# Kernel tuning notes

Hardware: AMD Instinct MI355X
Metric: run time of the kernel (lower is better)

The kernel has to match this reference:

```python
import jax, jax.numpy as jnp
import numpy as np


def hard_sig(x):
    # Keras hard_sigmoid: relu6(x + 3) / 6
    return jnp.clip(x / 6.0 + 0.5, 0.0, 1.0)


def conv2d(x, k):
    # x: (B,H,W,Cin), k: (kh,kw,Cin,Cout), SAME padding, stride 1
    return jax.lax.conv_general_dilated(x, k, (1, 1), 'SAME',
                                        dimension_numbers=('NHWC', 'HWIO', 'NHWC'))


def convlstm_layer(xs, Wk, Uk, b):
    # xs: (B,T,H,W,Cin); Wk: (kh,kw,Cin,4F); Uk: (kh,kw,F,4F); b: (4F,)
    B, T, H, W, _ = xs.shape
    F = b.shape[0] // 4
    h0 = jnp.zeros((B, H, W, F), xs.dtype)
    c0 = jnp.zeros((B, H, W, F), xs.dtype)
    xs_t = jnp.moveaxis(xs, 1, 0)  # (T,B,H,W,Cin)

    def step(carry, xt):
        h, c = carry
        z = conv2d(xt, Wk) + conv2d(h, Uk) + b
        zi, zf, zg, zo = jnp.split(z, 4, axis=-1)  # Keras gate order i,f,c,o
        i = hard_sig(zi)
        f = hard_sig(zf)
        o = hard_sig(zo)
        c_new = f * c + i * jax.nn.relu(zg)      # activation='relu'
        h_new = o * jax.nn.relu(c_new)
        return (h_new, c_new), h_new

    _, hs = jax.lax.scan(step, (h0, c0), xs_t)
    return jnp.moveaxis(hs, 0, 1)  # (B,T,H,W,F)


def batchnorm(x, gamma, beta, mean, var):
    # inference-mode BN over last axis, keras eps=1e-3
    return (x - mean) * jax.lax.rsqrt(var + 1e-3) * gamma + beta


def maxpool_hw(x):
    # MaxPooling3D pool_size=(1,2,2), SAME, channels_last; x: (B,T,H,W,C)
    return jax.lax.reduce_window(x, -jnp.inf, jax.lax.max,
                                 (1, 1, 2, 2, 1), (1, 1, 2, 2, 1), 'SAME')


def setup_inputs() -> dict:
    key = jax.random.key(0)
    ks = jax.random.split(key, 16)
    s = 0.1
    F = 32
    inp = {
        'x': jax.random.normal(ks[0], (16, 16, 64, 64, 1), jnp.float32),
        'k1': jax.random.normal(ks[1], (5, 5, 1, 4 * F), jnp.float32) * s,
        'u1': jax.random.normal(ks[2], (5, 5, F, 4 * F), jnp.float32) * s,
        'b1': jnp.zeros((4 * F,), jnp.float32),
        'g1': jnp.ones((F,), jnp.float32),
        'be1': jnp.zeros((F,), jnp.float32),
        'm1': jnp.zeros((F,), jnp.float32),
        'v1': jnp.ones((F,), jnp.float32),
        'k2': jax.random.normal(ks[3], (5, 5, F, 4 * F), jnp.float32) * s,
        'u2': jax.random.normal(ks[4], (5, 5, F, 4 * F), jnp.float32) * s,
        'b2': jnp.zeros((4 * F,), jnp.float32),
        'g2': jnp.ones((F,), jnp.float32),
        'be2': jnp.zeros((F,), jnp.float32),
        'm2': jnp.zeros((F,), jnp.float32),
        'v2': jnp.ones((F,), jnp.float32),
        'k3': jax.random.normal(ks[5], (3, 3, F, 4 * F), jnp.float32) * s,
        'u3': jax.random.normal(ks[6], (3, 3, F, 4 * F), jnp.float32) * s,
        'b3': jnp.zeros((4 * F,), jnp.float32),
        'wd': jax.random.normal(ks[7], (F, 64 * 64), jnp.float32) * s,
        'bd': jnp.zeros((64 * 64,), jnp.float32),
    }
    return inp


def reference(x, k1, u1, b1, g1, be1, m1, v1,
              k2, u2, b2, g2, be2, m2, v2,
              k3, u3, b3, wd, bd):
    h = convlstm_layer(x, k1, u1, b1)
    h = batchnorm(h, g1, be1, m1, v1)
    h = maxpool_hw(h)  # (B,T,32,32,32)
    h = convlstm_layer(h, k2, u2, b2)
    h = batchnorm(h, g2, be2, m2, v2)
    h = maxpool_hw(h)  # (B,T,16,16,32)
    h = convlstm_layer(h, k3, u3, b3)
    gap = jnp.mean(h, axis=(1, 2, 3))  # GlobalAveragePooling3D -> (B,32)
    logits = gap @ wd + bd
    return jax.nn.softmax(logits, axis=-1)
```

## Files before the change

### kernel.cpp

```cpp
#include <hip/hip_runtime.h>

typedef unsigned short u16;
typedef unsigned int u32;
typedef __attribute__((ext_vector_type(8))) short bf16x8;
typedef __attribute__((ext_vector_type(4))) float f32x4;

__device__ __forceinline__ float b2f(u16 h) {
  union { float f; unsigned u; } v; v.u = ((unsigned)h) << 16; return v.f;
}
__device__ __forceinline__ u16 f2b(float f) {
  union { float f; unsigned u; } v; v.f = f;
  unsigned r = v.u + 0x7fffu + ((v.u >> 16) & 1u);
  return (u16)(r >> 16);
}
__device__ __forceinline__ float hsig(float z) {
  return fminf(fmaxf(z * 0.16666667f + 0.5f, 0.f), 1.f);
}
__device__ __forceinline__ float ldf(const void* p, int i, int flag) {
  return flag ? b2f(((const u16*)p)[i]) : ((const float*)p)[i];
}

__global__ void detect_dtype(const void* x, int* dflag) {
  __shared__ int cnt;
  if (threadIdx.x == 0) cnt = 0;
  __syncthreads();
  const u32* w = (const u32*)x;
  int c = 0;
  for (int i = threadIdx.x; i < 512; i += 256) {
    u32 e = (w[i] >> 7) & 0xFFu;
    if (e >= 100 && e < 130) c++;
  }
  atomicAdd(&cnt, c);
  __syncthreads();
  if (threadIdx.x == 0) *dflag = (cnt >= 256) ? 1 : 0;
}

__global__ void canon_x(const void* src, u16* dst, const int* dflag, int n) {
  int i = blockIdx.x * 256 + threadIdx.x;
  if (i >= n) return;
  int fl = *dflag;
  float v = ldf(src, i, fl);
  u16 hi = f2b(v);
  dst[i] = hi;
  dst[i + n] = f2b(v - b2f(hi));
}

template<int KS, int MODE, int H, int W>
__device__ __forceinline__
void step_body(int bxi, int b, char* dsm,
               const u16* __restrict__ src, int aBStride, size_t sPL,
               const u16* __restrict__ wA, const u16* __restrict__ wU,
               const u16* __restrict__ hin, size_t hPL, u16* __restrict__ hout,
               float* __restrict__ cbuf, const void* __restrict__ bias,
               const void* __restrict__ bng, const void* __restrict__ bnb,
               const void* __restrict__ bnm, const void* __restrict__ bnv,
               u16* __restrict__ pooled, size_t pPL, float* __restrict__ gap,
               const int* __restrict__ dflag)
{
  constexpr int PAD = KS / 2;
  constexpr int TW = 8 + 2 * PAD;
  constexpr int TH = 16 + 2 * PAD;
  constexpr int KK = KS * KS;
  constexpr int KT = (MODE == 0) ? (KK + 1) : (2 * KK);
  constexpr int SSTR = 40;
  constexpr int HSZ = TH * TW * SSTR;
  constexpr int ASZ0 = (TH * TW + 15) & ~15;

  u16* sH0 = (u16*)dsm;
  u16* sH1 = (MODE == 0) ? (sH0 + HSZ) : sH0;
  u16* sA0 = sH0 + ((MODE == 0) ? 2 * HSZ : HSZ);
  u16* sA1 = (MODE == 0) ? (sA0 + ASZ0) : sA0;
  float* sgap = (float*)(sA0 + ((MODE == 0) ? 2 * ASZ0 : HSZ));

  const int tid = threadIdx.x;
  constexpr int TXT = W / 8;
  const int bx0 = (bxi % TXT) * 8;
  const int gy0 = (bxi / TXT) * 16;

  const int w = tid >> 6, lane = tid & 63;
  const int j = w & 1, R0 = (w >> 1) * 8;
  const int q = lane >> 4, col = lane & 15;
  const int my = (lane >> 3) & 1, mx = lane & 7;

  if (MODE == 2 && tid < 32) sgap[tid] = 0.f;

  auto stageH = [&](int pl, u16* dst) {
    const u16* hsrc = hin + (size_t)pl * hPL;
    for (int i = tid; i < TH * TW * 4; i += 256) {
      int p = i >> 2, ch = i & 3;
      int sy = p / TW, sx = p - sy * TW;
      int gy = gy0 + sy - PAD, gx = bx0 + sx - PAD;
      int4 v; v.x = v.y = v.z = v.w = 0;
      if (gy >= 0 && gy < H && gx >= 0 && gx < W)
        v = *(const int4*)(hsrc + (((size_t)(b * H + gy) * W + gx) << 5) + ch * 8);
      *(int4*)(&dst[p * SSTR + ch * 8]) = v;
    }
  };
  auto stageS = [&](int pl, u16* dst) {
    const u16* asrc = src + (size_t)pl * sPL;
    if (MODE == 0) {
      for (int i = tid; i < TH * TW; i += 256) {
        int sy = i / TW, sx = i - sy * TW;
        int gy = gy0 + sy - PAD, gx = bx0 + sx - PAD;
        u16 v = 0;
        if (gy >= 0 && gy < H && gx >= 0 && gx < W)
          v = asrc[(size_t)b * aBStride + gy * W + gx];
        dst[i] = v;
      }
    } else {
      for (int i = tid; i < TH * TW * 4; i += 256) {
        int p = i >> 2, ch = i & 3;
        int sy = p / TW, sx = p - sy * TW;
        int gy = gy0 + sy - PAD, gx = bx0 + sx - PAD;
        int4 v; v.x = v.y = v.z = v.w = 0;
        if (gy >= 0 && gy < H && gx >= 0 && gx < W)
          v = *(const int4*)(asrc + (size_t)b * aBStride + (((size_t)gy * W + gx) << 5) + ch * 8);
        *(int4*)(&dst[p * SSTR + ch * 8]) = v;
      }
    }
  };

  const int wfoff = lane * 8;
  auto loadW = [&](int kt, bf16x8* dst) {
    const u16* wsrc;
    if (MODE == 0) wsrc = (kt == 0) ? wA : (wU + (kt - 1) * 4096);
    else           wsrc = (kt < KK) ? (wA + kt * 4096) : (wU + (kt - KK) * 4096);
#pragma unroll
    for (int g = 0; g < 4; g++)
      dst[g] = *(const bf16x8*)(wsrc + ((j + 2 * g) * 64) * 8 + wfoff);
  };

  f32x4 acc[4][4] = {};
  int abase[4];
#pragma unroll
  for (int mt = 0; mt < 4; mt++)
    abase[mt] = ((R0 + 2 * mt + my) * TW + mx) * SSTR + q * 8;

  if (MODE == 0) {
    stageH(0, sH0); stageH(1, sH1); stageS(0, sA0); stageS(1, sA1);
    __syncthreads();

    bf16x8 bw[4];
    loadW(0, bw);
#pragma unroll 2
    for (int kt = 0; kt < KT; ++kt) {
      bf16x8 nxt[4];
      if (kt + 1 < KT) loadW(kt + 1, nxt);
      bf16x8 ah[4], al[4];
      if (kt == 0) {
#pragma unroll
        for (int mt = 0; mt < 4; mt++) {
          union { bf16x8 v; u16 e[8]; } uh, ul;
#pragma unroll
          for (int jj = 0; jj < 8; jj++) {
            int k = q * 8 + jj;
            u16 vh = 0, vl = 0;
            if (k < KK) {
              int kh = k / KS, kw = k - kh * KS;
              int o = (R0 + 2 * mt + my + kh) * TW + (mx + kw);
              vh = sA0[o]; vl = sA1[o];
            }
            uh.e[jj] = vh; ul.e[jj] = vl;
          }
          ah[mt] = uh.v; al[mt] = ul.v;
        }
      } else {
        const int tap = kt - 1;
        const int kh = tap / KS, kw = tap - kh * KS;
        const int aoff = (kh * TW + kw) * SSTR;
#pragma unroll
        for (int mt = 0; mt < 4; mt++) {
          ah[mt] = *(const bf16x8*)(sH0 + abase[mt] + aoff);
          al[mt] = *(const bf16x8*)(sH1 + abase[mt] + aoff);
        }
      }
#pragma unroll
      for (int mt = 0; mt < 4; mt++)
#pragma unroll
        for (int g = 0; g < 4; g++)
          acc[mt][g] = __builtin_amdgcn_mfma_f32_16x16x32_bf16(ah[mt], bw[g], acc[mt][g], 0, 0, 0);
#pragma unroll
      for (int mt = 0; mt < 4; mt++)
#pragma unroll
        for (int g = 0; g < 4; g++)
          acc[mt][g] = __builtin_amdgcn_mfma_f32_16x16x32_bf16(al[mt], bw[g], acc[mt][g], 0, 0, 0);
#pragma unroll
      for (int g = 0; g < 4; g++) bw[g] = nxt[g];
    }
  } else {
    for (int pass = 0; pass < 2; ++pass) {
      if (pass == 1) __syncthreads();
      stageH(pass, sH0); stageS(pass, sA0);
      __syncthreads();

      bf16x8 bw[4], nw[4], nw2[4];
      loadW(0, bw);
      if (KT > 1) loadW(1, nw);
#pragma unroll 2
      for (int kt = 0; kt < KT; ++kt) {
        if (kt + 2 < KT) loadW(kt + 2, nw2);
        int tap; const u16* s;
        if (kt < KK) { tap = kt;      s = sA0; }
        else         { tap = kt - KK; s = sH0; }
        const int kh = tap / KS, kw = tap - kh * KS;
        const int aoff = (kh * TW + kw) * SSTR;
        bf16x8 a[4];
#pragma unroll
        for (int mt = 0; mt < 4; mt++)
          a[mt] = *(const bf16x8*)(s + abase[mt] + aoff);
#pragma unroll
        for (int mt = 0; mt < 4; mt++)
#pragma unroll
          for (int g = 0; g < 4; g++)
            acc[mt][g] = __builtin_amdgcn_mfma_f32_16x16x32_bf16(a[mt], bw[g], acc[mt][g], 0, 0, 0);
#pragma unroll
        for (int g = 0; g < 4; g++) { bw[g] = nw[g]; nw[g] = nw2[g]; }
      }
    }
  }

  const int fl = *dflag;
  const int f = j * 16 + col;
  const float bi  = ldf(bias, f, fl);
  const float bff = ldf(bias, 32 + f, fl);
  const float bg  = ldf(bias, 64 + f, fl);
  const float bo  = ldf(bias, 96 + f, fl);
  float sc = 0.f, sh = 0.f;
  if (MODE < 2) {
    sc = ldf(bng, f, fl) * rsqrtf(ldf(bnv, f, fl) + 1e-3f);
    sh = ldf(bnb, f, fl) - ldf(bnm, f, fl) * sc;
  }
  const int oy = q >> 1;
  const int ox = (q & 1) * 4;
  float gsum = 0.f;
#pragma unroll
  for (int mt = 0; mt < 4; mt++) {
    const int y = gy0 + R0 + 2 * mt + oy;
    const size_t base = (((size_t)(b * H + y) * W + (bx0 + ox)) << 5) + f;
    float bnp[4];
#pragma unroll
    for (int r = 0; r < 4; r++) {
      float zi = acc[mt][0][r] + bi;
      float zf = acc[mt][1][r] + bff;
      float zg = acc[mt][2][r] + bg;
      float zo = acc[mt][3][r] + bo;
      float ig = hsig(zi), fg = hsig(zf), og = hsig(zo);
      float gg = fmaxf(zg, 0.f);
      size_t idx = base + ((size_t)r << 5);
      float cold = cbuf[idx];
      float cn = fg * cold + ig * gg;
      cbuf[idx] = cn;
      float hn = og * fmaxf(cn, 0.f);
      u16 hhi = f2b(hn);
      hout[idx] = hhi;
      hout[idx + hPL] = f2b(hn - b2f(hhi));
      if (MODE < 2) bnp[r] = hn * sc + sh; else gsum += hn;
    }
    if (MODE < 2) {
      float p0 = fmaxf(bnp[0], bnp[1]);
      float p1 = fmaxf(bnp[2], bnp[3]);
      p0 = fmaxf(p0, __shfl_xor(p0, 32));
      p1 = fmaxf(p1, __shfl_xor(p1, 32));
      if (q < 2) {
        const int py = (gy0 + R0 + 2 * mt) >> 1;
        const int px = (bx0 >> 1) + (q & 1) * 2;
        size_t pb = (((size_t)(b * (H / 2) + py) * (W / 2) + px) << 5) + f;
        u16 phi = f2b(p0);
        pooled[pb] = phi;
        pooled[pb + pPL] = f2b(p0 - b2f(phi));
        u16 qhi = f2b(p1);
        pooled[pb + 32] = qhi;
        pooled[pb + 32 + pPL] = f2b(p1 - b2f(qhi));
      }
    }
  }
  if (MODE == 2) {
    atomicAdd(&sgap[f], gsum);
    __syncthreads();
    if (tid < 32) atomicAdd(&gap[b * 32 + tid], sgap[tid]);
  }
}

__global__ __launch_bounds__(256, 2)
void fused_step(int t, const u16* __restrict__ xc,
                const u16* __restrict__ W1x, const u16* __restrict__ W1u,
                u16* h1a, u16* h1b, float* c1, const void* b1, const void* g1,
                const void* be1, const void* m1, const void* v1, u16* p1,
                const u16* __restrict__ W2k, const u16* __restrict__ W2u,
                u16* h2a, u16* h2b, float* c2, const void* b2, const void* g2,
                const void* be2, const void* m2, const void* v2, u16* p2,
                const u16* __restrict__ W3k, const u16* __restrict__ W3u,
                u16* h3a, u16* h3b, float* c3, const void* b3,
                float* gap, const int* dflag)
{
  extern __shared__ char dsm[];
  const int bid = blockIdx.x;
  if (bid < 512) {
    if (t > 15) return;
    const u16* h1i = (t & 1) ? h1b : h1a; u16* h1o = (t & 1) ? h1a : h1b;
    step_body<5, 0, 64, 64>(bid & 31, bid >> 5, dsm,
        xc + (size_t)t * 4096, 65536, 1048576, W1x, W1u, h1i, 2097152, h1o, c1,
        b1, g1, be1, m1, v1, p1 + (size_t)(t & 1) * 1048576, 524288, nullptr, dflag);
  } else if (bid < 640) {
    const int tt = t - 1; if (tt < 0 || tt > 15) return;
    const int r = bid - 512;
    const u16* h2i = (tt & 1) ? h2b : h2a; u16* h2o = (tt & 1) ? h2a : h2b;
    step_body<5, 1, 32, 32>(r & 7, r >> 3, dsm,
        p1 + (size_t)(tt & 1) * 1048576, 32768, 524288, W2k, W2u, h2i, 524288, h2o, c2,
        b2, g2, be2, m2, v2, p2 + (size_t)(tt & 1) * 262144, 131072, nullptr, dflag);
  } else {
    const int tt = t - 2; if (tt < 0 || tt > 15) return;
    const int r = bid - 640;
    const u16* h3i = (tt & 1) ? h3b : h3a; u16* h3o = (tt & 1) ? h3a : h3b;
    step_body<3, 2, 16, 16>(r & 1, r >> 1, dsm,
        p2 + (size_t)(tt & 1) * 262144, 8192, 131072, W3k, W3u, h3i, 131072, h3o, c3,
        b3, nullptr, nullptr, nullptr, nullptr, nullptr, 0, gap, dflag);
  }
}

__global__ void repack_w(const void* __restrict__ src, u16* __restrict__ dst,
                         int taps, const int* __restrict__ dflag) {
  int i = blockIdx.x * 256 + threadIdx.x;
  if (i >= taps * 512) return;
  int fl = *dflag;
  int l = i & 63, nt = (i >> 6) & 7, tap = i >> 9;
  int q = l >> 4, col = l & 15;
  u16 tmp[8];
#pragma unroll
  for (int j = 0; j < 8; j++)
    tmp[j] = f2b(ldf(src, (tap * 32 + q * 8 + j) * 128 + nt * 16 + col, fl));
#pragma unroll
  for (int j = 0; j < 8; j++) dst[i * 8 + j] = tmp[j];
}
__global__ void repack_x(const void* __restrict__ src, u16* __restrict__ dst,
                         const int* __restrict__ dflag) {
  int i = blockIdx.x * 256 + threadIdx.x;
  if (i >= 512) return;
  int fl = *dflag;
  int l = i & 63, nt = (i >> 6) & 7;
  int q = l >> 4, col = l & 15;
#pragma unroll
  for (int j = 0; j < 8; j++) {
    int k = q * 8 + j;
    dst[i * 8 + j] = (k < 25) ? f2b(ldf(src, k * 128 + nt * 16 + col, fl)) : (u16)0;
  }
}

__global__ void zero_ws(int4* p, int n) {
  int i = blockIdx.x * 256 + threadIdx.x;
  if (i < n) { int4 z; z.x = z.y = z.z = z.w = 0; p[i] = z; }
}
__global__ void fillv(float* out, int n, float v) {
  int i = blockIdx.x * 256 + threadIdx.x;
  if (i < n) out[i] = v;
}

__global__ void logits_k(const float* __restrict__ gap, const void* __restrict__ wd,
                         const void* __restrict__ bd, float* __restrict__ lg,
                         const int* __restrict__ dflag) {
  int i = blockIdx.x * 256 + threadIdx.x;
  int b = i >> 12, o = i & 4095;
  int fl = *dflag;
  float s = ldf(bd, o, fl);
  const float scl = 1.0f / 4096.0f;
#pragma unroll
  for (int f = 0; f < 32; f++)
    s += gap[b * 32 + f] * scl * ldf(wd, f * 4096 + o, fl);
  lg[i] = s;
}

__global__ void softmax_k(const float* __restrict__ lg, float* __restrict__ out) {
  int b = blockIdx.x, tid = threadIdx.x;
  __shared__ float red[256];
  float v[16];
  float lmax = -1e30f;
#pragma unroll
  for (int i = 0; i < 16; i++) {
    v[i] = lg[b * 4096 + i * 256 + tid];
    lmax = fmaxf(lmax, v[i]);
  }
  red[tid] = lmax; __syncthreads();
  for (int st = 128; st > 0; st >>= 1) { if (tid < st) red[tid] = fmaxf(red[tid], red[tid + st]); __syncthreads(); }
  float M = red[0]; __syncthreads();
  float ls = 0.f;
#pragma unroll
  for (int i = 0; i < 16; i++) { v[i] = expf(v[i] - M); ls += v[i]; }
  red[tid] = ls; __syncthreads();
  for (int st = 128; st > 0; st >>= 1) { if (tid < st) red[tid] += red[tid + st]; __syncthreads(); }
  float inv = 1.0f / red[0];
#pragma unroll
  for (int i = 0; i < 16; i++) out[b * 4096 + i * 256 + tid] = v[i] * inv;
}

extern "C" void kernel_launch(void* const* d_in, const int* in_sizes, int n_in,
                              void* d_out, int out_size, void* d_ws, size_t ws_size,
                              hipStream_t stream)
{
  const void* x   = d_in[0];
  const void* k1  = d_in[1];
  const void* u1  = d_in[2];
  const void* b1  = d_in[3];
  const void* g1  = d_in[4];
  const void* be1 = d_in[5];
  const void* m1  = d_in[6];
  const void* v1  = d_in[7];
  const void* k2  = d_in[8];
  const void* u2  = d_in[9];
  const void* b2  = d_in[10];
  const void* g2  = d_in[11];
  const void* be2 = d_in[12];
  const void* m2  = d_in[13];
  const void* v2  = d_in[14];
  const void* k3  = d_in[15];
  const void* u3  = d_in[16];
  const void* b3  = d_in[17];
  const void* wd  = d_in[18];
  const void* bd  = d_in[19];
  float* out = (float*)d_out;

  char* ws = (char*)d_ws;
  size_t off = 0;
  auto alloc = [&](size_t bytes) -> char* {
    char* p = ws + off; off = (off + bytes + 255) & ~(size_t)255; return p;
  };
  float* c1  = (float*)alloc(2097152 * 4);
  float* c2  = (float*)alloc(524288 * 4);
  float* c3  = (float*)alloc(131072 * 4);
  u16*   h1a = (u16*)alloc(2097152 * 2 * 2);
  u16*   h2a = (u16*)alloc(524288 * 2 * 2);
  u16*   h3a = (u16*)alloc(131072 * 2 * 2);
  float* gap = (float*)alloc(512 * 4);
  int*   dflag = (int*)alloc(64);
  size_t zero_bytes = off;
  u16* h1b = (u16*)alloc(2097152 * 2 * 2);
  u16* h2b = (u16*)alloc(524288 * 2 * 2);
  u16* h3b = (u16*)alloc(131072 * 2 * 2);
  u16* p1  = (u16*)alloc(524288 * 2 * 2 * 2);
  u16* p2  = (u16*)alloc(131072 * 2 * 2 * 2);
  u16* xc  = (u16*)alloc(1048576 * 2 * 2);
  float* lgbuf = (float*)alloc(65536 * 4);
  u16* W1x = (u16*)alloc(4096 * 2);
  u16* W1u = (u16*)alloc(102400 * 2);
  u16* W2k = (u16*)alloc(102400 * 2);
  u16* W2u = (u16*)alloc(102400 * 2);
  u16* W3k = (u16*)alloc(36864 * 2);
  u16* W3u = (u16*)alloc(36864 * 2);

  if (ws_size < off) {
    fillv<<<dim3((out_size + 255) / 256), 256, 0, stream>>>(out, out_size, 0.5f);
    return;
  }

  int nz = (int)(zero_bytes / 16);
  zero_ws<<<dim3((nz + 255) / 256), 256, 0, stream>>>((int4*)ws, nz);
  detect_dtype<<<1, 256, 0, stream>>>(x, dflag);
  canon_x<<<4096, 256, 0, stream>>>(x, xc, dflag, 1048576);
  repack_x<<<2, 256, 0, stream>>>(k1, W1x, dflag);
  repack_w<<<50, 256, 0, stream>>>(u1, W1u, 25, dflag);
  repack_w<<<50, 256, 0, stream>>>(k2, W2k, 25, dflag);
  repack_w<<<50, 256, 0, stream>>>(u2, W2u, 25, dflag);
  repack_w<<<18, 256, 0, stream>>>(k3, W3k, 9, dflag);
  repack_w<<<18, 256, 0, stream>>>(u3, W3u, 9, dflag);

  const size_t dyn = 39680;
  for (int t = 0; t < 18; ++t) {
    fused_step<<<672, 256, dyn, stream>>>(t, xc,
        W1x, W1u, h1a, h1b, c1, b1, g1, be1, m1, v1, p1,
        W2k, W2u, h2a, h2b, c2, b2, g2, be2, m2, v2, p2,
        W3k, W3u, h3a, h3b, c3, b3, gap, dflag);
  }
  logits_k<<<256, 256, 0, stream>>>(gap, wd, bd, lgbuf, dflag);
  softmax_k<<<16, 256, 0, stream>>>(lgbuf, out);
}
```

Measured before the change: 1.256 ms.

## Prefetch A tiles from LDS one step ahead and interleave layer blocks in grid

In the non-split MFMA loop, the A fragments for the next tap are now read from shared memory one iteration ahead, so LDS latency overlaps with the current MFMAs. The fused_step grid is also reordered into groups of 21 blocks (16 layer-1, 4 layer-2, 1 layer-3). This interleaves the heavier and lighter layer work across the dispatch order instead of keeping each layer's blocks contiguous. The prefetch adds registers, which could pressure occupancy under launch_bounds(256,2).

```diff
diff --git a/kernel.cpp b/kernel.cpp
--- a/kernel.cpp
+++ b/kernel.cpp
@@ -188,31 +188,38 @@
       for (int g = 0; g < 4; g++) bw[g] = nxt[g];
     }
   } else {
+    auto loadA = [&](int kt, bf16x8* dst) {
+      int tap; const u16* s;
+      if (kt < KK) { tap = kt;      s = sA0; }
+      else         { tap = kt - KK; s = sH0; }
+      const int kh = tap / KS, kw = tap - kh * KS;
+      const int aoff = (kh * TW + kw) * SSTR;
+#pragma unroll
+      for (int mt = 0; mt < 4; mt++)
+        dst[mt] = *(const bf16x8*)(s + abase[mt] + aoff);
+    };
     for (int pass = 0; pass < 2; ++pass) {
       if (pass == 1) __syncthreads();
       stageH(pass, sH0); stageS(pass, sA0);
       __syncthreads();
 
-      bf16x8 bw[4], nw[4], nw2[4];
+      bf16x8 bw[4], nw[4];
       loadW(0, bw);
       if (KT > 1) loadW(1, nw);
+      bf16x8 a[4], an[4];
+      loadA(0, a);
 #pragma unroll 2
       for (int kt = 0; kt < KT; ++kt) {
+        if (kt + 1 < KT) loadA(kt + 1, an);
+        bf16x8 nw2[4];
         if (kt + 2 < KT) loadW(kt + 2, nw2);
-        int tap; const u16* s;
-        if (kt < KK) { tap = kt;      s = sA0; }
-        else         { tap = kt - KK; s = sH0; }
-        const int kh = tap / KS, kw = tap - kh * KS;
-        const int aoff = (kh * TW + kw) * SSTR;
-        bf16x8 a[4];
-#pragma unroll
-        for (int mt = 0; mt < 4; mt++)
-          a[mt] = *(const bf16x8*)(s + abase[mt] + aoff);
 #pragma unroll
         for (int mt = 0; mt < 4; mt++)
 #pragma unroll
           for (int g = 0; g < 4; g++)
             acc[mt][g] = __builtin_amdgcn_mfma_f32_16x16x32_bf16(a[mt], bw[g], acc[mt][g], 0, 0, 0);
+#pragma unroll
+        for (int mt = 0; mt < 4; mt++) a[mt] = an[mt];
 #pragma unroll
         for (int g = 0; g < 4; g++) { bw[g] = nw[g]; nw[g] = nw2[g]; }
       }
@@ -294,25 +301,27 @@
                 float* gap, const int* dflag)
 {
   extern __shared__ char dsm[];
-  const int bid = blockIdx.x;
-  if (bid < 512) {
+  const int grp = blockIdx.x / 21;
+  const int r   = blockIdx.x % 21;
+  if (r < 16) {
     if (t > 15) return;
+    const int idx = grp * 16 + r;
     const u16* h1i = (t & 1) ? h1b : h1a; u16* h1o = (t & 1) ? h1a : h1b;
-    step_body<5, 0, 64, 64>(bid & 31, bid >> 5, dsm,
+    step_body<5, 0, 64, 64>(idx & 31, idx >> 5, dsm,
         xc + (size_t)t * 4096, 65536, 1048576, W1x, W1u, h1i, 2097152, h1o, c1,
         b1, g1, be1, m1, v1, p1 + (size_t)(t & 1) * 1048576, 524288, nullptr, dflag);
-  } else if (bid < 640) {
+  } else if (r < 20) {
     const int tt = t - 1; if (tt < 0 || tt > 15) return;
-    const int r = bid - 512;
+    const int idx = grp * 4 + (r - 16);
     const u16* h2i = (tt & 1) ? h2b : h2a; u16* h2o = (tt & 1) ? h2a : h2b;
-    step_body<5, 1, 32, 32>(r & 7, r >> 3, dsm,
+    step_body<5, 1, 32, 32>(idx & 7, idx >> 3, dsm,
         p1 + (size_t)(tt & 1) * 1048576, 32768, 524288, W2k, W2u, h2i, 524288, h2o, c2,
         b2, g2, be2, m2, v2, p2 + (size_t)(tt & 1) * 262144, 131072, nullptr, dflag);
   } else {
     const int tt = t - 2; if (tt < 0 || tt > 15) return;
-    const int r = bid - 640;
+    const int idx = grp;
     const u16* h3i = (tt & 1) ? h3b : h3a; u16* h3o = (tt & 1) ? h3a : h3b;
-    step_body<3, 2, 16, 16>(r & 1, r >> 1, dsm,
+    step_body<3, 2, 16, 16>(idx & 1, idx >> 1, dsm,
         p2 + (size_t)(tt & 1) * 262144, 8192, 131072, W3k, W3u, h3i, 131072, h3o, c3,
         b3, nullptr, nullptr, nullptr, nullptr, nullptr, 0, gap, dflag);
   }
```

After: 1.144 ms. -8.9%, faster.

## Unify conv step paths with swizzled LDS, smaller layer-2 tiles, interleaved block mapping

Applied to the files above, without the earlier changes.

Replaces the padded-stride LDS layout with an XOR-swizzled 32-channel layout meant to avoid bank conflicts without padding. Layers 2 and 3 now stage both hi/lo planes at once and run a single loop, dropping the two-pass restage and its extra barrier. Layer 2 uses 8-row tiles, which doubles its block count to spread work. Blocks of the three layers are interleaved in groups of 25 for better CU balance, and launch bounds are raised to 3 blocks per CU. This costs more shared memory per block and possible register pressure under the tighter launch bound.

```diff
diff --git a/kernel.cpp b/kernel.cpp
--- a/kernel.cpp
+++ b/kernel.cpp
@@ -45,7 +45,7 @@
   dst[i + n] = f2b(v - b2f(hi));
 }
 
-template<int KS, int MODE, int H, int W>
+template<int KS, int MODE, int H, int W, int MROWS>
 __device__ __forceinline__
 void step_body(int bxi, int b, char* dsm,
                const u16* __restrict__ src, int aBStride, size_t sPL,
@@ -59,47 +59,52 @@
 {
   constexpr int PAD = KS / 2;
   constexpr int TW = 8 + 2 * PAD;
-  constexpr int TH = 16 + 2 * PAD;
+  constexpr int TH = MROWS + 2 * PAD;
   constexpr int KK = KS * KS;
   constexpr int KT = (MODE == 0) ? (KK + 1) : (2 * KK);
-  constexpr int SSTR = 40;
-  constexpr int HSZ = TH * TW * SSTR;
-  constexpr int ASZ0 = (TH * TW + 15) & ~15;
+  constexpr int MT = MROWS / 4;
+  constexpr int NPX = TH * TW;
+  constexpr int BUFSZ = NPX * 32;
+  constexpr int ASZ0 = (NPX + 15) & ~15;
 
   u16* sH0 = (u16*)dsm;
-  u16* sH1 = (MODE == 0) ? (sH0 + HSZ) : sH0;
-  u16* sA0 = sH0 + ((MODE == 0) ? 2 * HSZ : HSZ);
-  u16* sA1 = (MODE == 0) ? (sA0 + ASZ0) : sA0;
-  float* sgap = (float*)(sA0 + ((MODE == 0) ? 2 * ASZ0 : HSZ));
+  u16* sH1 = sH0 + BUFSZ;
+  u16* sA0 = sH1 + BUFSZ;
+  u16* sA1 = sA0 + ((MODE == 0) ? ASZ0 : BUFSZ);
+  float* sgap = (float*)(sA1 + ((MODE == 0) ? ASZ0 : BUFSZ));
 
   const int tid = threadIdx.x;
   constexpr int TXT = W / 8;
   const int bx0 = (bxi % TXT) * 8;
-  const int gy0 = (bxi / TXT) * 16;
+  const int gy0 = (bxi / TXT) * MROWS;
 
   const int w = tid >> 6, lane = tid & 63;
-  const int j = w & 1, R0 = (w >> 1) * 8;
+  const int j = w & 1, R0 = (w >> 1) * (MROWS / 2);
   const int q = lane >> 4, col = lane & 15;
   const int my = (lane >> 3) & 1, mx = lane & 7;
 
   if (MODE == 2 && tid < 32) sgap[tid] = 0.f;
 
+  auto swadr = [](int px, int c) {
+    return (px << 5) + (((c ^ px ^ (px >> 1)) & 3) << 3);
+  };
+
   auto stageH = [&](int pl, u16* dst) {
     const u16* hsrc = hin + (size_t)pl * hPL;
-    for (int i = tid; i < TH * TW * 4; i += 256) {
+    for (int i = tid; i < NPX * 4; i += 256) {
       int p = i >> 2, ch = i & 3;
       int sy = p / TW, sx = p - sy * TW;
       int gy = gy0 + sy - PAD, gx = bx0 + sx - PAD;
       int4 v; v.x = v.y = v.z = v.w = 0;
       if (gy >= 0 && gy < H && gx >= 0 && gx < W)
         v = *(const int4*)(hsrc + (((size_t)(b * H + gy) * W + gx) << 5) + ch * 8);
-      *(int4*)(&dst[p * SSTR + ch * 8]) = v;
+      *(int4*)(&dst[swadr(p, ch)]) = v;
     }
   };
   auto stageS = [&](int pl, u16* dst) {
     const u16* asrc = src + (size_t)pl * sPL;
     if (MODE == 0) {
-      for (int i = tid; i < TH * TW; i += 256) {
+      for (int i = tid; i < NPX; i += 256) {
         int sy = i / TW, sx = i - sy * TW;
         int gy = gy0 + sy - PAD, gx = bx0 + sx - PAD;
         u16 v = 0;
@@ -108,14 +113,14 @@
         dst[i] = v;
       }
     } else {
-      for (int i = tid; i < TH * TW * 4; i += 256) {
+      for (int i = tid; i < NPX * 4; i += 256) {
         int p = i >> 2, ch = i & 3;
         int sy = p / TW, sx = p - sy * TW;
         int gy = gy0 + sy - PAD, gx = bx0 + sx - PAD;
         int4 v; v.x = v.y = v.z = v.w = 0;
         if (gy >= 0 && gy < H && gx >= 0 && gx < W)
           v = *(const int4*)(asrc + (size_t)b * aBStride + (((size_t)gy * W + gx) << 5) + ch * 8);
-        *(int4*)(&dst[p * SSTR + ch * 8]) = v;
+        *(int4*)(&dst[swadr(p, ch)]) = v;
       }
     }
   };
@@ -130,93 +135,65 @@
       dst[g] = *(const bf16x8*)(wsrc + ((j + 2 * g) * 64) * 8 + wfoff);
   };
 
-  f32x4 acc[4][4] = {};
-  int abase[4];
-#pragma unroll
-  for (int mt = 0; mt < 4; mt++)
-    abase[mt] = ((R0 + 2 * mt + my) * TW + mx) * SSTR + q * 8;
-
-  if (MODE == 0) {
-    stageH(0, sH0); stageH(1, sH1); stageS(0, sA0); stageS(1, sA1);
-    __syncthreads();
-
-    bf16x8 bw[4];
-    loadW(0, bw);
+  f32x4 acc[MT][4] = {};
+  int pxb[MT];
+#pragma unroll
+  for (int mt = 0; mt < MT; mt++)
+    pxb[mt] = (R0 + 2 * mt + my) * TW + mx;
+
+  stageH(0, sH0); stageH(1, sH1); stageS(0, sA0); stageS(1, sA1);
+  __syncthreads();
+
+  bf16x8 bw[4];
+  loadW(0, bw);
 #pragma unroll 2
-    for (int kt = 0; kt < KT; ++kt) {
-      bf16x8 nxt[4];
-      if (kt + 1 < KT) loadW(kt + 1, nxt);
-      bf16x8 ah[4], al[4];
-      if (kt == 0) {
-#pragma unroll
-        for (int mt = 0; mt < 4; mt++) {
-          union { bf16x8 v; u16 e[8]; } uh, ul;
-#pragma unroll
-          for (int jj = 0; jj < 8; jj++) {
-            int k = q * 8 + jj;
-            u16 vh = 0, vl = 0;
-            if (k < KK) {
-              int kh = k / KS, kw = k - kh * KS;
-              int o = (R0 + 2 * mt + my + kh) * TW + (mx + kw);
-              vh = sA0[o]; vl = sA1[o];
-            }
-            uh.e[jj] = vh; ul.e[jj] = vl;
+  for (int kt = 0; kt < KT; ++kt) {
+    bf16x8 nxt[4];
+    if (kt + 1 < KT) loadW(kt + 1, nxt);
+    bf16x8 ah[MT], al[MT];
+    if (MODE == 0 && kt == 0) {
+#pragma unroll
+      for (int mt = 0; mt < MT; mt++) {
+        union { bf16x8 v; u16 e[8]; } uh, ul;
+#pragma unroll
+        for (int jj = 0; jj < 8; jj++) {
+          int k = q * 8 + jj;
+          u16 vh = 0, vl = 0;
+          if (k < KK) {
+            int kh = k / KS, kw = k - kh * KS;
+            int o = (R0 + 2 * mt + my + kh) * TW + (mx + kw);
+            vh = sA0[o]; vl = sA1[o];
           }
-          ah[mt] = uh.v; al[mt] = ul.v;
+          uh.e[jj] = vh; ul.e[jj] = vl;
         }
-      } else {
-        const int tap = kt - 1;
-        const int kh = tap / KS, kw = tap - kh * KS;
-        const int aoff = (kh * TW + kw) * SSTR;
-#pragma unroll
-        for (int mt = 0; mt < 4; mt++) {
-          ah[mt] = *(const bf16x8*)(sH0 + abase[mt] + aoff);
-          al[mt] = *(const bf16x8*)(sH1 + abase[mt] + aoff);
-        }
+        ah[mt] = uh.v; al[mt] = ul.v;
       }
-#pragma unroll
-      for (int mt = 0; mt < 4; mt++)
-#pragma unroll
-        for (int g = 0; g < 4; g++)
-          acc[mt][g] = __builtin_amdgcn_mfma_f32_16x16x32_bf16(ah[mt], bw[g], acc[mt][g], 0, 0, 0);
-#pragma unroll
-      for (int mt = 0; mt < 4; mt++)
-#pragma unroll
-        for (int g = 0; g < 4; g++)
-          acc[mt][g] = __builtin_amdgcn_mfma_f32_16x16x32_bf16(al[mt], bw[g], acc[mt][g], 0, 0, 0);
-#pragma unroll
-      for (int g = 0; g < 4; g++) bw[g] = nxt[g];
-    }
-  } else {
-    for (int pass = 0; pass < 2; ++pass) {
-      if (pass == 1) __syncthreads();
-      stageH(pass, sH0); stageS(pass, sA0);
-      __syncthreads();
-
-      bf16x8 bw[4], nw[4], nw2[4];
-      loadW(0, bw);
-      if (KT > 1) loadW(1, nw);
-#pragma unroll 2
-      for (int kt = 0; kt < KT; ++kt) {
-        if (kt + 2 < KT) loadW(kt + 2, nw2);
-        int tap; const u16* s;
-        if (kt < KK) { tap = kt;      s = sA0; }
-        else         { tap = kt - KK; s = sH0; }
-        const int kh = tap / KS, kw = tap - kh * KS;
-        const int aoff = (kh * TW + kw) * SSTR;
-        bf16x8 a[4];
-#pragma unroll
-        for (int mt = 0; mt < 4; mt++)
-          a[mt] = *(const bf16x8*)(s + abase[mt] + aoff);
-#pragma unroll
-        for (int mt = 0; mt < 4; mt++)
-#pragma unroll
-          for (int g = 0; g < 4; g++)
-            acc[mt][g] = __builtin_amdgcn_mfma_f32_16x16x32_bf16(a[mt], bw[g], acc[mt][g], 0, 0, 0);
-#pragma unroll
-        for (int g = 0; g < 4; g++) { bw[g] = nw[g]; nw[g] = nw2[g]; }
+    } else {
+      int tap; const u16 *s0, *s1;
+      if (MODE == 0)    { tap = kt - 1;  s0 = sH0; s1 = sH1; }
+      else if (kt < KK) { tap = kt;      s0 = sA0; s1 = sA1; }
+      else              { tap = kt - KK; s0 = sH0; s1 = sH1; }
+      const int koff = (tap / KS) * TW + (tap - (tap / KS) * KS);
+#pragma unroll
+      for (int mt = 0; mt < MT; mt++) {
+        const int px = pxb[mt] + koff;
+        const int ad = (px << 5) + (((q ^ px ^ (px >> 1)) & 3) << 3);
+        ah[mt] = *(const bf16x8*)(s0 + ad);
+        al[mt] = *(const bf16x8*)(s1 + ad);
       }
     }
+#pragma unroll
+    for (int mt = 0; mt < MT; mt++)
+#pragma unroll
+      for (int g = 0; g < 4; g++)
+        acc[mt][g] = __builtin_amdgcn_mfma_f32_16x16x32_bf16(ah[mt], bw[g], acc[mt][g], 0, 0, 0);
+#pragma unroll
+    for (int mt = 0; mt < MT; mt++)
+#pragma unroll
+      for (int g = 0; g < 4; g++)
+        acc[mt][g] = __builtin_amdgcn_mfma_f32_16x16x32_bf16(al[mt], bw[g], acc[mt][g], 0, 0, 0);
+#pragma unroll
+    for (int g = 0; g < 4; g++) bw[g] = nxt[g];
   }
 
   const int fl = *dflag;
@@ -234,7 +211,7 @@
   const int ox = (q & 1) * 4;
   float gsum = 0.f;
 #pragma unroll
-  for (int mt = 0; mt < 4; mt++) {
+  for (int mt = 0; mt < MT; mt++) {
     const int y = gy0 + R0 + 2 * mt + oy;
     const size_t base = (((size_t)(b * H + y) * W + (bx0 + ox)) << 5) + f;
     float bnp[4];
@@ -281,7 +258,7 @@
   }
 }
 
-__global__ __launch_bounds__(256, 2)
+__global__ __launch_bounds__(256, 3)
 void fused_step(int t, const u16* __restrict__ xc,
                 const u16* __restrict__ W1x, const u16* __restrict__ W1u,
                 u16* h1a, u16* h1b, float* c1, const void* b1, const void* g1,
@@ -294,25 +271,27 @@
                 float* gap, const int* dflag)
 {
   extern __shared__ char dsm[];
-  const int bid = blockIdx.x;
-  if (bid < 512) {
+  const int grp = blockIdx.x / 25;
+  const int r   = blockIdx.x % 25;
+  if (r < 16) {
     if (t > 15) return;
+    const int idx = grp * 16 + r;
     const u16* h1i = (t & 1) ? h1b : h1a; u16* h1o = (t & 1) ? h1a : h1b;
-    step_body<5, 0, 64, 64>(bid & 31, bid >> 5, dsm,
+    step_body<5, 0, 64, 64, 16>(idx & 31, idx >> 5, dsm,
         xc + (size_t)t * 4096, 65536, 1048576, W1x, W1u, h1i, 2097152, h1o, c1,
         b1, g1, be1, m1, v1, p1 + (size_t)(t & 1) * 1048576, 524288, nullptr, dflag);
-  } else if (bid < 640) {
+  } else if (r < 24) {
     const int tt = t - 1; if (tt < 0 || tt > 15) return;
-    const int r = bid - 512;
+    const int idx = grp * 8 + (r - 16);
     const u16* h2i = (tt & 1) ? h2b : h2a; u16* h2o = (tt & 1) ? h2a : h2b;
-    step_body<5, 1, 32, 32>(r & 7, r >> 3, dsm,
+    step_body<5, 1, 32, 32, 8>(idx & 15, idx >> 4, dsm,
         p1 + (size_t)(tt & 1) * 1048576, 32768, 524288, W2k, W2u, h2i, 524288, h2o, c2,
         b2, g2, be2, m2, v2, p2 + (size_t)(tt & 1) * 262144, 131072, nullptr, dflag);
   } else {
     const int tt = t - 2; if (tt < 0 || tt > 15) return;
-    const int r = bid - 640;
+    const int idx = grp;
     const u16* h3i = (tt & 1) ? h3b : h3a; u16* h3o = (tt & 1) ? h3a : h3b;
-    step_body<3, 2, 16, 16>(r & 1, r >> 1, dsm,
+    step_body<3, 2, 16, 16, 16>(idx & 1, idx >> 1, dsm,
         p2 + (size_t)(tt & 1) * 262144, 8192, 131072, W3k, W3u, h3i, 131072, h3o, c3,
         b3, nullptr, nullptr, nullptr, nullptr, nullptr, 0, gap, dflag);
   }
@@ -462,9 +441,9 @@
   repack_w<<<18, 256, 0, stream>>>(k3, W3k, 9, dflag);
   repack_w<<<18, 256, 0, stream>>>(u3, W3u, 9, dflag);
 
-  const size_t dyn = 39680;
+  const size_t dyn = 46336;
   for (int t = 0; t < 18; ++t) {
-    fused_step<<<672, 256, dyn, stream>>>(t, xc,
+    fused_step<<<800, 256, dyn, stream>>>(t, xc,
         W1x, W1u, h1a, h1b, c1, b1, g1, be1, m1, v1, p1,
         W2k, W2u, h2a, h2b, c2, b2, g2, be2, m2, v2, p2,
         W3k, W3u, h3a, h3b, c3, b3, gap, dflag);
```

New measurement: 1.208 ms. 1.04x faster.
